# Kernel optimization log

Hardware: AMD Instinct MI355X
Metric: run time of the kernel (lower is better)

The kernel has to match this reference:

```python
import jax, jax.numpy as jnp
import numpy as np

B, L, D = 16, 1024, 256
H, FF = 8, 2048
DH = D // H
EPS = 1e-5


def setup_inputs() -> dict:
    key = jax.random.key(0)
    ks = jax.random.split(key, 13)
    s = 0.02
    return {
        "x": jax.random.normal(ks[0], (B, L, D), jnp.float32),
        "Wq": jax.random.normal(ks[1], (D, D), jnp.float32) * s,
        "bq": jnp.zeros((D,), jnp.float32),
        "Wk": jax.random.normal(ks[2], (D, D), jnp.float32) * s,
        "bk": jnp.zeros((D,), jnp.float32),
        "Wv": jax.random.normal(ks[3], (D, D), jnp.float32) * s,
        "bv": jnp.zeros((D,), jnp.float32),
        "Wo": jax.random.normal(ks[4], (D, D), jnp.float32) * s,
        "bo": jnp.zeros((D,), jnp.float32),
        "W1": jax.random.normal(ks[5], (D, FF), jnp.float32) * s,
        "b1": jnp.zeros((FF,), jnp.float32),
        "W2": jax.random.normal(ks[6], (FF, D), jnp.float32) * s,
        "b2": jnp.zeros((D,), jnp.float32),
        "g1": jnp.ones((D,), jnp.float32),
        "be1": jnp.zeros((D,), jnp.float32),
        "g2": jnp.ones((D,), jnp.float32),
        "be2": jnp.zeros((D,), jnp.float32),
    }


def _layernorm(x, g, b):
    m = jnp.mean(x, axis=-1, keepdims=True)
    v = jnp.mean(jnp.square(x - m), axis=-1, keepdims=True)
    return (x - m) * jax.lax.rsqrt(v + EPS) * g + b


def reference(x, Wq, bq, Wk, bk, Wv, bv, Wo, bo, W1, b1, W2, b2, g1, be1, g2, be2):
    b, l, d = x.shape
    # QKV projections, split heads (torch split/cat == reshape to [b,l,H,dh])
    q = (x @ Wq + bq).reshape(b, l, H, DH)
    k = (x @ Wk + bk).reshape(b, l, H, DH)
    v = (x @ Wv + bv).reshape(b, l, H, DH)
    # scaled dot-product attention per head
    scores = jnp.einsum("bqhd,bkhd->bhqk", q, k) / np.float32(DH) ** 0.5
    attn = jax.nn.softmax(scores, axis=-1)
    o = jnp.einsum("bhqk,bkhd->bqhd", attn, v).reshape(b, l, d)
    o = o @ Wo + bo
    # residual + LN1 (dropout p=0.0 -> identity)
    h = _layernorm(x + o, g1, be1)
    # FFN + residual + LN2
    ff = jax.nn.relu(h @ W1 + b1) @ W2 + b2
    return _layernorm(h + ff, g2, be2)
```

## Files before the change

kernel.cpp:

```cpp
#include <hip/hip_runtime.h>
#include <math.h>

#define B_  16
#define L_  1024
#define D_  256
#define H_  8
#define DH_ 32
#define FF_ 2048
#define NROW (B_*L_)
#define QKVS 768

typedef __attribute__((ext_vector_type(8))) short short8;
typedef __attribute__((ext_vector_type(4))) short short4v;
typedef __attribute__((ext_vector_type(4))) float f32x4;
typedef __attribute__((ext_vector_type(4))) unsigned uint4v;
typedef __attribute__((ext_vector_type(4))) unsigned short ushort4v;
typedef unsigned short ushortT;

__device__ inline ushortT f2bf(float f) {
    unsigned u = __builtin_bit_cast(unsigned, f);
    u += 0x7fffu + ((u >> 16) & 1u);
    return (ushortT)(u >> 16);
}

__device__ inline float bf2f(ushortT u) {
    return __builtin_bit_cast(float, (unsigned)u << 16);
}

__device__ inline float fexp2(float x) {
#if __has_builtin(__builtin_amdgcn_exp2f)
    return __builtin_amdgcn_exp2f(x);
#else
    return exp2f(x);
#endif
}

__device__ inline void gload_lds16(const ushortT* g, ushortT* l) {
    __builtin_amdgcn_global_load_lds(
        (const __attribute__((address_space(1))) unsigned*)g,
        (__attribute__((address_space(3))) unsigned*)l, 16, 0, 0);
}

__device__ inline unsigned lds_addr(const void* p) {
    return (unsigned)(size_t)(const __attribute__((address_space(3))) void*)p;
}

template<bool RELU, bool OBF16>
__global__ __launch_bounds__(256)
void gemm_bf16_kernel(const ushortT* __restrict__ A, const ushortT* __restrict__ Bt,
                      const float* __restrict__ bias, void* __restrict__ Cv,
                      int K, int ldb, int ldc)
{
    __shared__ ushortT As[2][128 * 32];
    __shared__ ushortT Bs[2][128 * 32];

    const int tid   = threadIdx.x;
    const int w     = tid >> 6;
    const int lane  = tid & 63;
    const int qlane = lane & 15;
    const int g     = lane >> 4;
    const int wm    = w >> 1, wn = w & 1;
    const int m0    = (blockIdx.x & 127) * 128;
    const int n0    = (blockIdx.x >> 7) * 128;

    int srowA[2], sq[2];
    #pragma unroll
    for (int j = 0; j < 2; ++j) {
        int idx = (j * 4 + w) * 64 + lane;
        srowA[j] = idx >> 2;
        sq[j]    = (idx & 3) ^ (srowA[j] & 3);
    }
    const int rsw = (g ^ (qlane & 3)) * 8;

    f32x4 acc[4][4];
    #pragma unroll
    for (int mi = 0; mi < 4; ++mi)
        #pragma unroll
        for (int ni = 0; ni < 4; ++ni)
            acc[mi][ni] = (f32x4){0.f, 0.f, 0.f, 0.f};

    auto stage = [&](int buf, int kt) {
        const int k0 = kt * 32;
        #pragma unroll
        for (int j = 0; j < 2; ++j) {
            gload_lds16(A + (size_t)(m0 + srowA[j]) * K + k0 + sq[j] * 8,
                        &As[buf][(j * 4 + w) * 512]);
            gload_lds16(Bt + (size_t)(n0 + srowA[j]) * ldb + k0 + sq[j] * 8,
                        &Bs[buf][(j * 4 + w) * 512]);
        }
    };

    stage(0, 0);
    __syncthreads();

    const int nt = K >> 5;
    for (int t = 0; t < nt; ++t) {
        const int cur = t & 1;
        if (t + 1 < nt) stage(cur ^ 1, t + 1);

        short8 af[4], bfr[4];
        #pragma unroll
        for (int mi = 0; mi < 4; ++mi)
            af[mi] = *(const short8*)&As[cur][(wm * 64 + mi * 16 + qlane) * 32 + rsw];
        #pragma unroll
        for (int ni = 0; ni < 4; ++ni)
            bfr[ni] = *(const short8*)&Bs[cur][(wn * 64 + ni * 16 + qlane) * 32 + rsw];

        #pragma unroll
        for (int mi = 0; mi < 4; ++mi)
            #pragma unroll
            for (int ni = 0; ni < 4; ++ni)
                acc[mi][ni] = __builtin_amdgcn_mfma_f32_16x16x32_bf16(
                    af[mi], bfr[ni], acc[mi][ni], 0, 0, 0);

        __syncthreads();
    }

    #pragma unroll
    for (int mi = 0; mi < 4; ++mi) {
        #pragma unroll
        for (int ni = 0; ni < 4; ++ni) {
            const int n = n0 + wn * 64 + ni * 16 + qlane;
            const float bval = bias ? bias[n] : 0.f;
            #pragma unroll
            for (int r = 0; r < 4; ++r) {
                const int m = m0 + wm * 64 + mi * 16 + 4 * g + r;
                float v = acc[mi][ni][r] + bval;
                if (RELU)  v = fmaxf(v, 0.f);
                if (OBF16) ((ushortT*)Cv)[(size_t)m * ldc + n] = f2bf(v);
                else       ((float*)Cv)[(size_t)m * ldc + n] = v;
            }
        }
    }
}

template<bool RELU, bool OBF16>
__global__ __launch_bounds__(512)
void gemm_big_kernel(const ushortT* __restrict__ A, const ushortT* __restrict__ Bt,
                     const float* __restrict__ bias, void* __restrict__ Cv,
                     int K, int ldb, int ldc, int mtiles)
{
    __shared__ ushortT As[2][256 * 32];
    __shared__ ushortT Bs[2][128 * 32];

    const int tid   = threadIdx.x;
    const int w     = tid >> 6;
    const int lane  = tid & 63;
    const int qlane = lane & 15;
    const int g     = lane >> 4;
    const int wm    = w >> 1, wn = w & 1;
    const int m0    = (blockIdx.x & (mtiles - 1)) * 256;
    const int n0    = (blockIdx.x / mtiles) * 128;

    const int rsw = (g ^ (qlane & 3)) * 8;

    f32x4 acc[4][4];
    #pragma unroll
    for (int mi = 0; mi < 4; ++mi)
        #pragma unroll
        for (int ni = 0; ni < 4; ++ni)
            acc[mi][ni] = (f32x4){0.f, 0.f, 0.f, 0.f};

    auto stage = [&](int buf, int kt) {
        const int k0 = kt * 32;
        #pragma unroll
        for (int j = 0; j < 2; ++j) {
            const int c = j * 512 + tid;
            const int row = c >> 2, kq = (c & 3) ^ (row & 3);
            gload_lds16(A + (size_t)(m0 + row) * K + k0 + kq * 8,
                        &As[buf][c * 8]);
        }
        {
            const int row = tid >> 2, kq = (tid & 3) ^ (row & 3);
            gload_lds16(Bt + (size_t)(n0 + row) * ldb + k0 + kq * 8,
                        &Bs[buf][tid * 8]);
        }
    };

    stage(0, 0);
    __syncthreads();

    const int nt = K >> 5;
    for (int t = 0; t < nt; ++t) {
        const int cur = t & 1;
        if (t + 1 < nt) stage(cur ^ 1, t + 1);

        short8 af[4], bfr[4];
        #pragma unroll
        for (int mi = 0; mi < 4; ++mi)
            af[mi] = *(const short8*)&As[cur][(wm * 64 + mi * 16 + qlane) * 32 + rsw];
        #pragma unroll
        for (int ni = 0; ni < 4; ++ni)
            bfr[ni] = *(const short8*)&Bs[cur][(wn * 64 + ni * 16 + qlane) * 32 + rsw];

        #pragma unroll
        for (int mi = 0; mi < 4; ++mi)
            #pragma unroll
            for (int ni = 0; ni < 4; ++ni)
                acc[mi][ni] = __builtin_amdgcn_mfma_f32_16x16x32_bf16(
                    af[mi], bfr[ni], acc[mi][ni], 0, 0, 0);

        __syncthreads();
    }

    #pragma unroll
    for (int mi = 0; mi < 4; ++mi) {
        #pragma unroll
        for (int ni = 0; ni < 4; ++ni) {
            const int n = n0 + wn * 64 + ni * 16 + qlane;
            const float bval = bias ? bias[n] : 0.f;
            #pragma unroll
            for (int r = 0; r < 4; ++r) {
                const int m = m0 + wm * 64 + mi * 16 + 4 * g + r;
                float v = acc[mi][ni][r] + bval;
                if (RELU)  v = fmaxf(v, 0.f);
                if (OBF16) ((ushortT*)Cv)[(size_t)m * ldc + n] = f2bf(v);
                else       ((float*)Cv)[(size_t)m * ldc + n] = v;
            }
        }
    }
}

template<bool OBF16>
__global__ __launch_bounds__(256)
void gemm64_kernel(const ushortT* __restrict__ A, const ushortT* __restrict__ Bt,
                   const float* __restrict__ bias, void* __restrict__ Cv, int K)
{
    __shared__ ushortT As[2][64 * 64];
    __shared__ ushortT Bs[2][64 * 64];

    const int tid   = threadIdx.x;
    const int w     = tid >> 6;
    const int lane  = tid & 63;
    const int qlane = lane & 15;
    const int g     = lane >> 4;
    const int bid   = blockIdx.x;
    const int m0    = (bid & 255) * 64;
    const int n0    = (bid >> 8) * 64;

    int srow[2], sq[2];
    #pragma unroll
    for (int j = 0; j < 2; ++j) {
        const int c = j * 256 + tid;
        srow[j] = c >> 3;
        sq[j]   = (c & 7) ^ (srow[j] & 7);
    }

    f32x4 acc[4];
    #pragma unroll
    for (int ni = 0; ni < 4; ++ni) acc[ni] = (f32x4){0.f, 0.f, 0.f, 0.f};

    auto stage = [&](int buf, int kt) {
        const int k0 = kt * 64;
        #pragma unroll
        for (int j = 0; j < 2; ++j) {
            gload_lds16(A + (size_t)(m0 + srow[j]) * K + k0 + sq[j] * 8,
                        &As[buf][(j * 256 + tid) * 8]);
            gload_lds16(Bt + (size_t)(n0 + srow[j]) * K + k0 + sq[j] * 8,
                        &Bs[buf][(j * 256 + tid) * 8]);
        }
    };

    stage(0, 0);
    __syncthreads();

    const int arow = w * 16 + qlane;
    const int nt = K >> 6;
    for (int t = 0; t < nt; ++t) {
        const int cur = t & 1;
        if (t + 1 < nt) stage(cur ^ 1, t + 1);

        #pragma unroll
        for (int ks = 0; ks < 2; ++ks) {
            const int aq = (ks * 4 + g) ^ (arow & 7);
            short8 af = *(const short8*)&As[cur][arow * 64 + aq * 8];
            #pragma unroll
            for (int ni = 0; ni < 4; ++ni) {
                const int brow = ni * 16 + qlane;
                const int bq = (ks * 4 + g) ^ (brow & 7);
                short8 bfr = *(const short8*)&Bs[cur][brow * 64 + bq * 8];
                acc[ni] = __builtin_amdgcn_mfma_f32_16x16x32_bf16(af, bfr, acc[ni], 0, 0, 0);
            }
        }

        __syncthreads();
    }

    #pragma unroll
    for (int ni = 0; ni < 4; ++ni) {
        const int n = n0 + ni * 16 + qlane;
        const float bval = bias[n];
        #pragma unroll
        for (int r = 0; r < 4; ++r) {
            const int m = m0 + w * 16 + 4 * g + r;
            float v = acc[ni][r] + bval;
            if (OBF16) ((ushortT*)Cv)[(size_t)m * D_ + n] = f2bf(v);
            else       ((float*)Cv)[(size_t)m * D_ + n] = v;
        }
    }
}

template<bool XF32, bool YF32, bool OBF16>
__global__ __launch_bounds__(256)
void ln_kernel(const void* __restrict__ X, const void* __restrict__ Y,
               const float* __restrict__ g, const float* __restrict__ bb,
               void* __restrict__ out)
{
    const int tid  = threadIdx.x;
    const int lane = tid & 63;
    const int w    = tid >> 6;
    const size_t row = (size_t)blockIdx.x * 4 + w;
    const int c    = lane * 4;

    float xv[4], yv[4];
    if (XF32) {
        float4 v = *reinterpret_cast<const float4*>((const float*)X + row * D_ + c);
        xv[0] = v.x; xv[1] = v.y; xv[2] = v.z; xv[3] = v.w;
    } else {
        ushort4v v = *reinterpret_cast<const ushort4v*>((const ushortT*)X + row * D_ + c);
        #pragma unroll
        for (int j = 0; j < 4; ++j) xv[j] = bf2f(v[j]);
    }
    if (YF32) {
        float4 v = *reinterpret_cast<const float4*>((const float*)Y + row * D_ + c);
        yv[0] = v.x; yv[1] = v.y; yv[2] = v.z; yv[3] = v.w;
    } else {
        ushort4v v = *reinterpret_cast<const ushort4v*>((const ushortT*)Y + row * D_ + c);
        #pragma unroll
        for (int j = 0; j < 4; ++j) yv[j] = bf2f(v[j]);
    }

    float s0 = xv[0] + yv[0], s1 = xv[1] + yv[1], s2 = xv[2] + yv[2], s3 = xv[3] + yv[3];

    float sum = s0 + s1 + s2 + s3;
    float sq  = s0 * s0 + s1 * s1 + s2 * s2 + s3 * s3;
    #pragma unroll
    for (int off = 1; off < 64; off <<= 1) {
        sum += __shfl_xor(sum, off);
        sq  += __shfl_xor(sq, off);
    }
    const float mean = sum * (1.f / D_);
    const float var  = sq * (1.f / D_) - mean * mean;
    const float rinv = rsqrtf(var + 1e-5f);

    const float4 gv = *reinterpret_cast<const float4*>(g + c);
    const float4 bv = *reinterpret_cast<const float4*>(bb + c);
    float o0 = (s0 - mean) * rinv * gv.x + bv.x;
    float o1 = (s1 - mean) * rinv * gv.y + bv.y;
    float o2 = (s2 - mean) * rinv * gv.z + bv.z;
    float o3 = (s3 - mean) * rinv * gv.w + bv.w;

    if (OBF16) {
        unsigned p0 = (unsigned)f2bf(o0) | ((unsigned)f2bf(o1) << 16);
        unsigned p1 = (unsigned)f2bf(o2) | ((unsigned)f2bf(o3) << 16);
        uint2 u = {p0, p1};
        *reinterpret_cast<uint2*>((ushortT*)out + row * D_ + c) = u;
    } else {
        float4 ov = {o0, o1, o2, o3};
        *reinterpret_cast<float4*>((float*)out + row * D_ + c) = ov;
    }
}

__global__ __launch_bounds__(512)
void attn_mfma_kernel(const ushortT* __restrict__ qkv, ushortT* __restrict__ o)
{
    __shared__ __align__(16) ushortT K4[2][2048];
    __shared__ __align__(16) ushortT Vs[2][2048];

    const int tid   = threadIdx.x;
    const int lane  = tid & 63;
    const int w     = tid >> 6;
    const int qlane = lane & 15;
    const int g     = lane >> 4;

    const int bid = blockIdx.x;
    const int bh  = bid & 127;
    const int b   = bh >> 3;
    const int h   = bh & 7;
    const int q0  = (bid >> 7) * 128;

    const size_t inbase = (size_t)b * L_ * QKVS + h * 32;
    const size_t obase  = (size_t)b * L_ * 256 + h * 32;

    const short8 qf = *(const short8*)(qkv + inbase + (size_t)(q0 + w * 16 + qlane) * QKVS + g * 8);

    f32x4 ot0 = {0.f, 0.f, 0.f, 0.f}, ot1 = {0.f, 0.f, 0.f, 0.f};
    float l_reg = 0.f;

    const float CEXP = 0.25503540f;

    const int t2   = tid & 255;
    const int skey = t2 >> 2;
    const int sg   = t2 & 3;
    const bool isK = tid < 256;
    const ushortT* src = qkv + inbase + (isK ? 256 : 512) + sg * 8 + (size_t)skey * QKVS;

    char* K4b = (char*)&K4[0][0];
    char* Vsb = (char*)&Vs[0][0];

    unsigned kwoff = (unsigned)sg * 1024u + (unsigned)skey * 16u;
    kwoff ^= (kwoff >> 5) & 0x60;
    const unsigned vwoff = ((unsigned)((skey >> 2) * 2 + (sg >> 1))) * 128u +
                           ((unsigned)(skey & 3)) * 32u +
                           ((((unsigned)(sg & 1)) ^ ((unsigned)(sg >> 1))) * 16u);
    char* wbase = isK ? K4b : Vsb;
    const unsigned woff = isK ? kwoff : vwoff;

    unsigned kroff[4];
    #pragma unroll
    for (int kt4 = 0; kt4 < 4; ++kt4) {
        unsigned off = (unsigned)g * 1024u + (unsigned)(kt4 * 16 + qlane) * 16u;
        kroff[kt4] = off ^ ((off >> 5) & 0x60);
    }
    const unsigned vrbase  = lds_addr(&Vs[0][0]) + 256u * (unsigned)g + 8u * (unsigned)qlane;
    const unsigned vrbase2 = vrbase ^ 64u;

    short8 reg = *(const short8*)src;

    #pragma unroll 2
    for (int t = 0; t < L_ / 64; ++t) {
        const unsigned bo = (unsigned)(t & 1) * 4096u;
        *(short8*)(wbase + bo + woff) = reg;
        if (t + 1 < L_ / 64)
            reg = *(const short8*)(src + (size_t)((t + 1) * 64) * QKVS);
        __syncthreads();

        f32x4 st[4];
        __builtin_amdgcn_s_setprio(1);
        #pragma unroll
        for (int kt4 = 0; kt4 < 4; ++kt4) {
            short8 kf = *(const short8*)(K4b + bo + kroff[kt4]);
            st[kt4] = __builtin_amdgcn_mfma_f32_16x16x32_bf16(kf, qf, (f32x4){0.f,0.f,0.f,0.f}, 0, 0, 0);
        }
        __builtin_amdgcn_s_setprio(0);

        float p[16];
        float s4[4];
        #pragma unroll
        for (int kt4 = 0; kt4 < 4; ++kt4) {
            #pragma unroll
            for (int r = 0; r < 4; ++r)
                p[kt4 * 4 + r] = fexp2(st[kt4][r] * CEXP);
            s4[kt4] = (p[kt4*4] + p[kt4*4+1]) + (p[kt4*4+2] + p[kt4*4+3]);
        }
        float ssum = (s4[0] + s4[1]) + (s4[2] + s4[3]);
        ssum += __shfl_xor(ssum, 16);
        ssum += __shfl_xor(ssum, 32);
        l_reg += ssum;

        unsigned pk_[8];
        #pragma unroll
        for (int i = 0; i < 8; ++i)
            asm("v_cvt_pk_bf16_f32 %0, %1, %2" : "=v"(pk_[i]) : "v"(p[2*i]), "v"(p[2*i+1]));
        const short8 pa0 = __builtin_bit_cast(short8, (uint4v){pk_[0], pk_[1], pk_[2], pk_[3]});
        const short8 pa1 = __builtin_bit_cast(short8, (uint4v){pk_[4], pk_[5], pk_[6], pk_[7]});

        const unsigned va  = vrbase  + bo;
        const unsigned va2 = vrbase2 + bo;
        __builtin_amdgcn_s_setprio(1);
        {
            short4v v00, v01, v10, v11;
            asm volatile("ds_read_b64_tr_b16 %0, %1"             : "=v"(v00) : "v"(va));
            asm volatile("ds_read_b64_tr_b16 %0, %1 offset:1024" : "=v"(v01) : "v"(va));
            asm volatile("ds_read_b64_tr_b16 %0, %1 offset:128"  : "=v"(v10) : "v"(va2));
            asm volatile("ds_read_b64_tr_b16 %0, %1 offset:1152" : "=v"(v11) : "v"(va2));
            asm volatile("s_waitcnt lgkmcnt(0)" ::: "memory");
            __builtin_amdgcn_sched_barrier(0);
            short8 vb0 = __builtin_shufflevector(v00, v01, 0,1,2,3,4,5,6,7);
            short8 vb1 = __builtin_shufflevector(v10, v11, 0,1,2,3,4,5,6,7);
            ot0 = __builtin_amdgcn_mfma_f32_16x16x32_bf16(pa0, vb0, ot0, 0, 0, 0);
            ot1 = __builtin_amdgcn_mfma_f32_16x16x32_bf16(pa0, vb1, ot1, 0, 0, 0);
        }
        {
            short4v v00, v01, v10, v11;
            asm volatile("ds_read_b64_tr_b16 %0, %1 offset:2048" : "=v"(v00) : "v"(va));
            asm volatile("ds_read_b64_tr_b16 %0, %1 offset:3072" : "=v"(v01) : "v"(va));
            asm volatile("ds_read_b64_tr_b16 %0, %1 offset:2176" : "=v"(v10) : "v"(va2));
            asm volatile("ds_read_b64_tr_b16 %0, %1 offset:3200" : "=v"(v11) : "v"(va2));
            asm volatile("s_waitcnt lgkmcnt(0)" ::: "memory");
            __builtin_amdgcn_sched_barrier(0);
            short8 vb0 = __builtin_shufflevector(v00, v01, 0,1,2,3,4,5,6,7);
            short8 vb1 = __builtin_shufflevector(v10, v11, 0,1,2,3,4,5,6,7);
            ot0 = __builtin_amdgcn_mfma_f32_16x16x32_bf16(pa1, vb0, ot0, 0, 0, 0);
            ot1 = __builtin_amdgcn_mfma_f32_16x16x32_bf16(pa1, vb1, ot1, 0, 0, 0);
        }
        __builtin_amdgcn_s_setprio(0);
    }

    const float linv = 1.f / l_reg;
    #pragma unroll
    for (int r = 0; r < 4; ++r) {
        float lr = __shfl(linv, 4 * g + r);
        size_t row = (size_t)(q0 + w * 16 + 4 * g + r);
        ushortT* op = o + obase + row * 256;
        op[qlane]      = f2bf(ot0[r] * lr);
        op[16 + qlane] = f2bf(ot1[r] * lr);
    }
}

__global__ __launch_bounds__(256)
void prep_kernel(const float* __restrict__ x, ushortT* __restrict__ xb,
                 const float* __restrict__ Wq, const float* __restrict__ Wk,
                 const float* __restrict__ Wv, const float* __restrict__ Wo,
                 ushortT* __restrict__ Wqkvb, ushortT* __restrict__ Wob,
                 const float* __restrict__ W1, ushortT* __restrict__ W1b,
                 const float* __restrict__ W2, ushortT* __restrict__ W2b,
                 const float* __restrict__ bq, const float* __restrict__ bk,
                 const float* __restrict__ bv, float* __restrict__ bqkv)
{
    __shared__ float t[32][33];
    const int bid = blockIdx.x;
    const int tid = threadIdx.x;

    if (bid < 4096) {
        const int i = (bid * 256 + tid) * 4;
        float4 v = *reinterpret_cast<const float4*>(x + i);
        unsigned p0 = (unsigned)f2bf(v.x) | ((unsigned)f2bf(v.y) << 16);
        unsigned p1 = (unsigned)f2bf(v.z) | ((unsigned)f2bf(v.w) << 16);
        uint2 u = {p0, p1};
        *reinterpret_cast<uint2*>(xb + i) = u;
        return;
    }
    int i = bid - 4096;
    const float* W; ushortT* Wt; int K, N, bx, by;
    if (i < 256) {
        const int which = i >> 6, j = i & 63;
        bx = j & 7; by = j >> 3; K = 256; N = 256;
        W  = which == 0 ? Wq : which == 1 ? Wk : which == 2 ? Wv : Wo;
        Wt = which == 0 ? Wqkvb : which == 1 ? Wqkvb + 65536
           : which == 2 ? Wqkvb + 131072 : Wob;
    } else if (i < 768) {
        const int j = i - 256; bx = j & 63; by = j >> 6; K = 256; N = 2048;
        W = W1; Wt = W1b;
    } else if (i < 1280) {
        const int j = i - 768; bx = j & 7; by = j >> 3; K = 2048; N = 256;
        W = W2; Wt = W2b;
    } else {
        for (int k = tid; k < 768; k += 256)
            bqkv[k] = k < 256 ? bq[k] : (k < 512 ? bk[k - 256] : bv[k - 512]);
        return;
    }
    const int tx = tid & 31, ty = tid >> 5;
    const int k0 = by * 32, n0 = bx * 32;
    #pragma unroll
    for (int r = ty; r < 32; r += 8) t[r][tx] = W[(size_t)(k0 + r) * N + n0 + tx];
    __syncthreads();
    #pragma unroll
    for (int r = ty; r < 32; r += 8) Wt[(size_t)(n0 + r) * K + k0 + tx] = f2bf(t[tx][r]);
}

extern "C" void kernel_launch(void* const* d_in, const int* in_sizes, int n_in,
                              void* d_out, int out_size, void* d_ws, size_t ws_size,
                              hipStream_t stream)
{
    const float* x   = (const float*)d_in[0];
    const float* Wq  = (const float*)d_in[1];
    const float* bq  = (const float*)d_in[2];
    const float* Wk  = (const float*)d_in[3];
    const float* bk  = (const float*)d_in[4];
    const float* Wv  = (const float*)d_in[5];
    const float* bv  = (const float*)d_in[6];
    const float* Wo  = (const float*)d_in[7];
    const float* bo  = (const float*)d_in[8];
    const float* W1  = (const float*)d_in[9];
    const float* b1  = (const float*)d_in[10];
    const float* W2  = (const float*)d_in[11];
    const float* b2  = (const float*)d_in[12];
    const float* g1  = (const float*)d_in[13];
    const float* be1 = (const float*)d_in[14];
    const float* g2  = (const float*)d_in[15];
    const float* be2 = (const float*)d_in[16];
    float* out = (float*)d_out;

    char* wsb = (char*)d_ws;
    const size_t MB = (size_t)1 << 20;
    ushortT* Wqkvb = (ushortT*)(wsb);
    ushortT* Wob   = (ushortT*)(wsb + 393216);
    ushortT* W1b   = (ushortT*)(wsb + 512 * 1024);
    ushortT* W2b   = (ushortT*)(wsb + 1536 * 1024);
    float*   bqkv  = (float*)  (wsb + 2560 * 1024);
    ushortT* xb  = (ushortT*)(wsb + 3 * MB);
    ushortT* qkv = (ushortT*)(wsb + 11 * MB);
    ushortT* ob  = (ushortT*)(wsb + 35 * MB);
    ushortT* ao  = (ushortT*)(wsb + 43 * MB);
    ushortT* hb  = (ushortT*)(wsb + 3 * MB);
    ushortT* f1  = (ushortT*)(wsb + 11 * MB);

    prep_kernel<<<dim3(5377), dim3(256), 0, stream>>>(
        x, xb, Wq, Wk, Wv, Wo, Wqkvb, Wob, W1, W1b, W2, W2b, bq, bk, bv, bqkv);

    gemm_bf16_kernel<false, true><<<dim3(768), dim3(256), 0, stream>>>(
        xb, Wqkvb, bqkv, qkv, 256, 256, QKVS);

    attn_mfma_kernel<<<dim3(1024), dim3(512), 0, stream>>>(qkv, ob);

    gemm64_kernel<true><<<dim3(1024), dim3(256), 0, stream>>>(ob, Wob, bo, ao, 256);

    ln_kernel<false, false, true><<<dim3(NROW / 4), dim3(256), 0, stream>>>(
        xb, ao, g1, be1, hb);

    gemm_big_kernel<true, true><<<dim3(1024), dim3(512), 0, stream>>>(
        hb, W1b, b1, f1, 256, 256, FF_, 64);

    gemm64_kernel<false><<<dim3(1024), dim3(256), 0, stream>>>(f1, W2b, b2, out, 2048);

    ln_kernel<false, true, false><<<dim3(NROW / 4), dim3(256), 0, stream>>>(
        hb, out, g2, be2, out);
}
```

Before: 132.1 us.

## Widen N=256 GEMM tiles to 64x128 and process 128 keys per attention barrier

The 64x64 GEMM used for the output projection and the FFN down-projection becomes a 64x128 tile: each wave computes a 32x64 sub-block with 2x4 MFMAs per k-step, and the grid is halved. Each A fragment is reused across more N, and fewer blocks re-read the same A rows. The attention kernel now stages two 64-key chunks per double-buffered step (128 keys), halving the number of __syncthreads in the key loop at the cost of doubled LDS and extra prefetch registers. The GEMM's LDS footprint and register pressure also grow, which may reduce occupancy.

```diff
diff --git a/kernel.cpp b/kernel.cpp
--- a/kernel.cpp
+++ b/kernel.cpp
@@ -223,48 +223,48 @@
 
 template<bool OBF16>
 __global__ __launch_bounds__(256)
-void gemm64_kernel(const ushortT* __restrict__ A, const ushortT* __restrict__ Bt,
-                   const float* __restrict__ bias, void* __restrict__ Cv, int K)
+void gemm_n128_kernel(const ushortT* __restrict__ A, const ushortT* __restrict__ Bt,
+                      const float* __restrict__ bias, void* __restrict__ Cv, int K)
 {
     __shared__ ushortT As[2][64 * 64];
-    __shared__ ushortT Bs[2][64 * 64];
+    __shared__ ushortT Bs[2][128 * 64];
 
     const int tid   = threadIdx.x;
     const int w     = tid >> 6;
     const int lane  = tid & 63;
     const int qlane = lane & 15;
     const int g     = lane >> 4;
+    const int wm    = w >> 1, wn = w & 1;
     const int bid   = blockIdx.x;
     const int m0    = (bid & 255) * 64;
-    const int n0    = (bid >> 8) * 64;
-
-    int srow[2], sq[2];
-    #pragma unroll
-    for (int j = 0; j < 2; ++j) {
-        const int c = j * 256 + tid;
-        srow[j] = c >> 3;
-        sq[j]   = (c & 7) ^ (srow[j] & 7);
-    }
-
-    f32x4 acc[4];
-    #pragma unroll
-    for (int ni = 0; ni < 4; ++ni) acc[ni] = (f32x4){0.f, 0.f, 0.f, 0.f};
+    const int n0    = (bid >> 8) * 128;
+
+    f32x4 acc[2][4];
+    #pragma unroll
+    for (int mi = 0; mi < 2; ++mi)
+        #pragma unroll
+        for (int ni = 0; ni < 4; ++ni)
+            acc[mi][ni] = (f32x4){0.f, 0.f, 0.f, 0.f};
 
     auto stage = [&](int buf, int kt) {
         const int k0 = kt * 64;
         #pragma unroll
         for (int j = 0; j < 2; ++j) {
-            gload_lds16(A + (size_t)(m0 + srow[j]) * K + k0 + sq[j] * 8,
-                        &As[buf][(j * 256 + tid) * 8]);
-            gload_lds16(Bt + (size_t)(n0 + srow[j]) * K + k0 + sq[j] * 8,
-                        &Bs[buf][(j * 256 + tid) * 8]);
+            const int c = j * 256 + tid;
+            const int row = c >> 3, q = (c & 7) ^ (row & 7);
+            gload_lds16(A + (size_t)(m0 + row) * K + k0 + q * 8, &As[buf][c * 8]);
+        }
+        #pragma unroll
+        for (int j = 0; j < 4; ++j) {
+            const int c = j * 256 + tid;
+            const int row = c >> 3, q = (c & 7) ^ (row & 7);
+            gload_lds16(Bt + (size_t)(n0 + row) * K + k0 + q * 8, &Bs[buf][c * 8]);
         }
     };
 
     stage(0, 0);
     __syncthreads();
 
-    const int arow = w * 16 + qlane;
     const int nt = K >> 6;
     for (int t = 0; t < nt; ++t) {
         const int cur = t & 1;
@@ -272,30 +272,43 @@
 
         #pragma unroll
         for (int ks = 0; ks < 2; ++ks) {
-            const int aq = (ks * 4 + g) ^ (arow & 7);
-            short8 af = *(const short8*)&As[cur][arow * 64 + aq * 8];
+            short8 af[2], bfr[4];
+            #pragma unroll
+            for (int mi = 0; mi < 2; ++mi) {
+                const int arow = wm * 32 + mi * 16 + qlane;
+                const int aq = (ks * 4 + g) ^ (arow & 7);
+                af[mi] = *(const short8*)&As[cur][arow * 64 + aq * 8];
+            }
             #pragma unroll
             for (int ni = 0; ni < 4; ++ni) {
-                const int brow = ni * 16 + qlane;
+                const int brow = wn * 64 + ni * 16 + qlane;
                 const int bq = (ks * 4 + g) ^ (brow & 7);
-                short8 bfr = *(const short8*)&Bs[cur][brow * 64 + bq * 8];
-                acc[ni] = __builtin_amdgcn_mfma_f32_16x16x32_bf16(af, bfr, acc[ni], 0, 0, 0);
-            }
+                bfr[ni] = *(const short8*)&Bs[cur][brow * 64 + bq * 8];
+            }
+            #pragma unroll
+            for (int mi = 0; mi < 2; ++mi)
+                #pragma unroll
+                for (int ni = 0; ni < 4; ++ni)
+                    acc[mi][ni] = __builtin_amdgcn_mfma_f32_16x16x32_bf16(
+                        af[mi], bfr[ni], acc[mi][ni], 0, 0, 0);
         }
 
         __syncthreads();
     }
 
     #pragma unroll
-    for (int ni = 0; ni < 4; ++ni) {
-        const int n = n0 + ni * 16 + qlane;
-        const float bval = bias[n];
-        #pragma unroll
-        for (int r = 0; r < 4; ++r) {
-            const int m = m0 + w * 16 + 4 * g + r;
-            float v = acc[ni][r] + bval;
-            if (OBF16) ((ushortT*)Cv)[(size_t)m * D_ + n] = f2bf(v);
-            else       ((float*)Cv)[(size_t)m * D_ + n] = v;
+    for (int mi = 0; mi < 2; ++mi) {
+        #pragma unroll
+        for (int ni = 0; ni < 4; ++ni) {
+            const int n = n0 + wn * 64 + ni * 16 + qlane;
+            const float bval = bias[n];
+            #pragma unroll
+            for (int r = 0; r < 4; ++r) {
+                const int m = m0 + wm * 32 + mi * 16 + 4 * g + r;
+                float v = acc[mi][ni][r] + bval;
+                if (OBF16) ((ushortT*)Cv)[(size_t)m * D_ + n] = f2bf(v);
+                else       ((float*)Cv)[(size_t)m * D_ + n] = v;
+            }
         }
     }
 }
@@ -364,8 +377,8 @@
 __global__ __launch_bounds__(512)
 void attn_mfma_kernel(const ushortT* __restrict__ qkv, ushortT* __restrict__ o)
 {
-    __shared__ __align__(16) ushortT K4[2][2048];
-    __shared__ __align__(16) ushortT Vs[2][2048];
+    __shared__ __align__(16) ushortT K4[2][2][2048];
+    __shared__ __align__(16) ushortT Vs[2][2][2048];
 
     const int tid   = threadIdx.x;
     const int lane  = tid & 63;
@@ -395,8 +408,8 @@
     const bool isK = tid < 256;
     const ushortT* src = qkv + inbase + (isK ? 256 : 512) + sg * 8 + (size_t)skey * QKVS;
 
-    char* K4b = (char*)&K4[0][0];
-    char* Vsb = (char*)&Vs[0][0];
+    char* K4b = (char*)&K4[0][0][0];
+    char* Vsb = (char*)&Vs[0][0][0];
 
     unsigned kwoff = (unsigned)sg * 1024u + (unsigned)skey * 16u;
     kwoff ^= (kwoff >> 5) & 0x60;
@@ -412,79 +425,88 @@
         unsigned off = (unsigned)g * 1024u + (unsigned)(kt4 * 16 + qlane) * 16u;
         kroff[kt4] = off ^ ((off >> 5) & 0x60);
     }
-    const unsigned vrbase  = lds_addr(&Vs[0][0]) + 256u * (unsigned)g + 8u * (unsigned)qlane;
+    const unsigned vrbase  = lds_addr(&Vs[0][0][0]) + 256u * (unsigned)g + 8u * (unsigned)qlane;
     const unsigned vrbase2 = vrbase ^ 64u;
 
-    short8 reg = *(const short8*)src;
-
-    #pragma unroll 2
-    for (int t = 0; t < L_ / 64; ++t) {
-        const unsigned bo = (unsigned)(t & 1) * 4096u;
-        *(short8*)(wbase + bo + woff) = reg;
-        if (t + 1 < L_ / 64)
-            reg = *(const short8*)(src + (size_t)((t + 1) * 64) * QKVS);
+    short8 reg0 = *(const short8*)src;
+    short8 reg1 = *(const short8*)(src + (size_t)64 * QKVS);
+
+    for (int t = 0; t < L_ / 128; ++t) {
+        const unsigned bo = (unsigned)(t & 1) * 8192u;
+        *(short8*)(wbase + bo + woff)         = reg0;
+        *(short8*)(wbase + bo + 4096u + woff) = reg1;
+        if (t + 1 < L_ / 128) {
+            const size_t roff = (size_t)((t + 1) * 128) * QKVS;
+            reg0 = *(const short8*)(src + roff);
+            reg1 = *(const short8*)(src + roff + (size_t)64 * QKVS);
+        }
         __syncthreads();
 
-        f32x4 st[4];
-        __builtin_amdgcn_s_setprio(1);
-        #pragma unroll
-        for (int kt4 = 0; kt4 < 4; ++kt4) {
-            short8 kf = *(const short8*)(K4b + bo + kroff[kt4]);
-            st[kt4] = __builtin_amdgcn_mfma_f32_16x16x32_bf16(kf, qf, (f32x4){0.f,0.f,0.f,0.f}, 0, 0, 0);
-        }
-        __builtin_amdgcn_s_setprio(0);
-
-        float p[16];
-        float s4[4];
-        #pragma unroll
-        for (int kt4 = 0; kt4 < 4; ++kt4) {
-            #pragma unroll
-            for (int r = 0; r < 4; ++r)
-                p[kt4 * 4 + r] = fexp2(st[kt4][r] * CEXP);
-            s4[kt4] = (p[kt4*4] + p[kt4*4+1]) + (p[kt4*4+2] + p[kt4*4+3]);
-        }
-        float ssum = (s4[0] + s4[1]) + (s4[2] + s4[3]);
-        ssum += __shfl_xor(ssum, 16);
-        ssum += __shfl_xor(ssum, 32);
-        l_reg += ssum;
-
-        unsigned pk_[8];
-        #pragma unroll
-        for (int i = 0; i < 8; ++i)
-            asm("v_cvt_pk_bf16_f32 %0, %1, %2" : "=v"(pk_[i]) : "v"(p[2*i]), "v"(p[2*i+1]));
-        const short8 pa0 = __builtin_bit_cast(short8, (uint4v){pk_[0], pk_[1], pk_[2], pk_[3]});
-        const short8 pa1 = __builtin_bit_cast(short8, (uint4v){pk_[4], pk_[5], pk_[6], pk_[7]});
-
-        const unsigned va  = vrbase  + bo;
-        const unsigned va2 = vrbase2 + bo;
-        __builtin_amdgcn_s_setprio(1);
-        {
-            short4v v00, v01, v10, v11;
-            asm volatile("ds_read_b64_tr_b16 %0, %1"             : "=v"(v00) : "v"(va));
-            asm volatile("ds_read_b64_tr_b16 %0, %1 offset:1024" : "=v"(v01) : "v"(va));
-            asm volatile("ds_read_b64_tr_b16 %0, %1 offset:128"  : "=v"(v10) : "v"(va2));
-            asm volatile("ds_read_b64_tr_b16 %0, %1 offset:1152" : "=v"(v11) : "v"(va2));
-            asm volatile("s_waitcnt lgkmcnt(0)" ::: "memory");
-            __builtin_amdgcn_sched_barrier(0);
-            short8 vb0 = __builtin_shufflevector(v00, v01, 0,1,2,3,4,5,6,7);
-            short8 vb1 = __builtin_shufflevector(v10, v11, 0,1,2,3,4,5,6,7);
-            ot0 = __builtin_amdgcn_mfma_f32_16x16x32_bf16(pa0, vb0, ot0, 0, 0, 0);
-            ot1 = __builtin_amdgcn_mfma_f32_16x16x32_bf16(pa0, vb1, ot1, 0, 0, 0);
-        }
-        {
-            short4v v00, v01, v10, v11;
-            asm volatile("ds_read_b64_tr_b16 %0, %1 offset:2048" : "=v"(v00) : "v"(va));
-            asm volatile("ds_read_b64_tr_b16 %0, %1 offset:3072" : "=v"(v01) : "v"(va));
-            asm volatile("ds_read_b64_tr_b16 %0, %1 offset:2176" : "=v"(v10) : "v"(va2));
-            asm volatile("ds_read_b64_tr_b16 %0, %1 offset:3200" : "=v"(v11) : "v"(va2));
-            asm volatile("s_waitcnt lgkmcnt(0)" ::: "memory");
-            __builtin_amdgcn_sched_barrier(0);
-            short8 vb0 = __builtin_shufflevector(v00, v01, 0,1,2,3,4,5,6,7);
-            short8 vb1 = __builtin_shufflevector(v10, v11, 0,1,2,3,4,5,6,7);
-            ot0 = __builtin_amdgcn_mfma_f32_16x16x32_bf16(pa1, vb0, ot0, 0, 0, 0);
-            ot1 = __builtin_amdgcn_mfma_f32_16x16x32_bf16(pa1, vb1, ot1, 0, 0, 0);
-        }
-        __builtin_amdgcn_s_setprio(0);
+        #pragma unroll
+        for (int sub = 0; sub < 2; ++sub) {
+            const unsigned so = bo + (unsigned)sub * 4096u;
+
+            f32x4 st[4];
+            __builtin_amdgcn_s_setprio(1);
+            #pragma unroll
+            for (int kt4 = 0; kt4 < 4; ++kt4) {
+                short8 kf = *(const short8*)(K4b + so + kroff[kt4]);
+                st[kt4] = __builtin_amdgcn_mfma_f32_16x16x32_bf16(kf, qf, (f32x4){0.f,0.f,0.f,0.f}, 0, 0, 0);
+            }
+            __builtin_amdgcn_s_setprio(0);
+
+            float p[16];
+            float s4[4];
+            #pragma unroll
+            for (int kt4 = 0; kt4 < 4; ++kt4) {
+                #pragma unroll
+                for (int r = 0; r < 4; ++r)
+                    p[kt4 * 4 + r] = fexp2(st[kt4][r] * CEXP);
+                s4[kt4] = (p[kt4*4] + p[kt4*4+1]) + (p[kt4*4+2] + p[kt4*4+3]);
+            }
+            float ssum = (s4[0] + s4[1]) + (s4[2] + s4[3]);
+            ssum += __shfl_xor(ssum, 16);
+            ssum += __shfl_xor(ssum, 32);
+            l_reg += ssum;
+
+            unsigned pk_[8];
+            #pragma unroll
+            for (int i = 0; i < 8; ++i)
+                asm("v_cvt_pk_bf16_f32 %0, %1, %2" : "=v"(pk_[i]) : "v"(p[2*i]), "v"(p[2*i+1]));
+            const short8 pa0 = __builtin_bit_cast(short8, (uint4v){pk_[0], pk_[1], pk_[2], pk_[3]});
+            const short8 pa1 = __builtin_bit_cast(short8, (uint4v){pk_[4], pk_[5], pk_[6], pk_[7]});
+
+            const unsigned va  = vrbase  + so;
+            const unsigned va2 = vrbase2 + so;
+            __builtin_amdgcn_s_setprio(1);
+            {
+                short4v v00, v01, v10, v11;
+                asm volatile("ds_read_b64_tr_b16 %0, %1"             : "=v"(v00) : "v"(va));
+                asm volatile("ds_read_b64_tr_b16 %0, %1 offset:1024" : "=v"(v01) : "v"(va));
+                asm volatile("ds_read_b64_tr_b16 %0, %1 offset:128"  : "=v"(v10) : "v"(va2));
+                asm volatile("ds_read_b64_tr_b16 %0, %1 offset:1152" : "=v"(v11) : "v"(va2));
+                asm volatile("s_waitcnt lgkmcnt(0)" ::: "memory");
+                __builtin_amdgcn_sched_barrier(0);
+                short8 vb0 = __builtin_shufflevector(v00, v01, 0,1,2,3,4,5,6,7);
+                short8 vb1 = __builtin_shufflevector(v10, v11, 0,1,2,3,4,5,6,7);
+                ot0 = __builtin_amdgcn_mfma_f32_16x16x32_bf16(pa0, vb0, ot0, 0, 0, 0);
+                ot1 = __builtin_amdgcn_mfma_f32_16x16x32_bf16(pa0, vb1, ot1, 0, 0, 0);
+            }
+            {
+                short4v v00, v01, v10, v11;
+                asm volatile("ds_read_b64_tr_b16 %0, %1 offset:2048" : "=v"(v00) : "v"(va));
+                asm volatile("ds_read_b64_tr_b16 %0, %1 offset:3072" : "=v"(v01) : "v"(va));
+                asm volatile("ds_read_b64_tr_b16 %0, %1 offset:2176" : "=v"(v10) : "v"(va2));
+                asm volatile("ds_read_b64_tr_b16 %0, %1 offset:3200" : "=v"(v11) : "v"(va2));
+                asm volatile("s_waitcnt lgkmcnt(0)" ::: "memory");
+                __builtin_amdgcn_sched_barrier(0);
+                short8 vb0 = __builtin_shufflevector(v00, v01, 0,1,2,3,4,5,6,7);
+                short8 vb1 = __builtin_shufflevector(v10, v11, 0,1,2,3,4,5,6,7);
+                ot0 = __builtin_amdgcn_mfma_f32_16x16x32_bf16(pa1, vb0, ot0, 0, 0, 0);
+                ot1 = __builtin_amdgcn_mfma_f32_16x16x32_bf16(pa1, vb1, ot1, 0, 0, 0);
+            }
+            __builtin_amdgcn_s_setprio(0);
+        }
     }
 
     const float linv = 1.f / l_reg;
@@ -594,7 +616,7 @@
 
     attn_mfma_kernel<<<dim3(1024), dim3(512), 0, stream>>>(qkv, ob);
 
-    gemm64_kernel<true><<<dim3(1024), dim3(256), 0, stream>>>(ob, Wob, bo, ao, 256);
+    gemm_n128_kernel<true><<<dim3(512), dim3(256), 0, stream>>>(ob, Wob, bo, ao, 256);
 
     ln_kernel<false, false, true><<<dim3(NROW / 4), dim3(256), 0, stream>>>(
         xb, ao, g1, be1, hb);
@@ -602,7 +624,7 @@
     gemm_big_kernel<true, true><<<dim3(1024), dim3(512), 0, stream>>>(
         hb, W1b, b1, f1, 256, 256, FF_, 64);
 
-    gemm64_kernel<false><<<dim3(1024), dim3(256), 0, stream>>>(f1, W2b, b2, out, 2048);
+    gemm_n128_kernel<false><<<dim3(512), dim3(256), 0, stream>>>(f1, W2b, b2, out, 2048);
 
     ln_kernel<false, true, false><<<dim3(NROW / 4), dim3(256), 0, stream>>>(
         hb, out, g2, be2, out);
```

New measurement: 137.4 us. 4.0% more time.
